# Kernel optimization log

Measured on AMD Instinct MI355X. Metric: run time of the kernel, lower is better.

Reference implementation:

```python
import jax, jax.numpy as jnp
import numpy as np

SEQDIM = 512      # hidden-state dim of h
EMBED_DIM = 512   # attention embedding dim
VFEAT_DIM = 384   # visual feature channels (must equal VFEAT_LEN for the broadcast in the original code)
VFEAT_LEN = 384   # number of visual regions


def setup_inputs() -> dict:
    key = jax.random.key(0)
    k_h, k_v, k_wh, k_wv, k_wg = jax.random.split(key, 5)
    h = jax.random.normal(k_h, (SEQDIM, 1), dtype=jnp.float32)
    v = jax.random.normal(k_v, (VFEAT_DIM, VFEAT_LEN), dtype=jnp.float32)
    wh = jax.random.normal(k_wh, (VFEAT_LEN, EMBED_DIM), dtype=jnp.float32) * 0.05
    wv = jax.random.normal(k_wv, (EMBED_DIM, VFEAT_DIM), dtype=jnp.float32) * 0.05
    wg = jax.random.normal(k_wg, (EMBED_DIM, SEQDIM), dtype=jnp.float32) * 0.05
    return {"h": h, "v": v, "wh": wh, "wv": wv, "wg": wg}


def reference(h, v, wh, wv, wg):
    # s = W_v V + (W_g h_t) 1^T  -> (embed_dim, vfeat_len)
    s = jnp.matmul(wv, v) + jnp.matmul(wg, h)  # (E, L) + (E, 1) broadcasts == outer product with ones row
    # z = w_h tanh(s)            -> (vfeat_len, vfeat_len)
    z = jnp.matmul(wh, jnp.tanh(s))
    alpha = jax.nn.softmax(z, axis=-1)
    # v (D, L) * alpha[..., None] (L, L, 1) -> broadcast to (L, D, L) with D == L
    weighted_avg = v * alpha[..., None]
    return weighted_avg
```

## Files before the change

### kernel.cpp

```cpp
#include <hip/hip_runtime.h>
#include <hip/hip_bf16.h>

#define SDIM 512
#define EDIM 512
#define LDIM 384
#define DDIM 384

typedef __attribute__((ext_vector_type(4))) float float4v;

__global__ __launch_bounds__(384) void k_tanh_s(
    const float* __restrict__ h, const float* __restrict__ v,
    const float* __restrict__ wv, const float* __restrict__ wg,
    float* __restrict__ t)
{
    const int e0  = blockIdx.x * 2;
    const int tid = threadIdx.x;
    __shared__ float wvs0[DDIM], wvs1[DDIM];
    __shared__ float red[2][6];

    float g0 = 0.f, g1 = 0.f;
    for (int k = tid; k < SDIM; k += 384) {
        const float hk = h[k];
        g0 += wg[e0 * SDIM + k] * hk;
        g1 += wg[(e0 + 1) * SDIM + k] * hk;
    }
    for (int off = 32; off > 0; off >>= 1) {
        g0 += __shfl_down(g0, off, 64);
        g1 += __shfl_down(g1, off, 64);
    }
    if ((tid & 63) == 0) { red[0][tid >> 6] = g0; red[1][tid >> 6] = g1; }

    wvs0[tid] = wv[e0 * DDIM + tid];
    wvs1[tid] = wv[(e0 + 1) * DDIM + tid];
    __syncthreads();

    const float gh0 = ((red[0][0] + red[0][1]) + (red[0][2] + red[0][3]))
                      + (red[0][4] + red[0][5]);
    const float gh1 = ((red[1][0] + red[1][1]) + (red[1][2] + red[1][3]))
                      + (red[1][4] + red[1][5]);

    const float* vp = v + tid;
    float a[4] = {0.f, 0.f, 0.f, 0.f};
    float b[4] = {0.f, 0.f, 0.f, 0.f};
    for (int kb = 0; kb < DDIM; kb += 16) {
        float vv[16];
        #pragma unroll
        for (int u = 0; u < 16; ++u)
            vv[u] = vp[(kb + u) * LDIM];
        #pragma unroll
        for (int u = 0; u < 16; ++u) {
            a[u & 3] += wvs0[kb + u] * vv[u];
            b[u & 3] += wvs1[kb + u] * vv[u];
        }
    }
    t[e0 * LDIM + tid]       = tanhf((a[0] + a[1]) + (a[2] + a[3]) + gh0);
    t[(e0 + 1) * LDIM + tid] = tanhf((b[0] + b[1]) + (b[2] + b[3]) + gh1);
}

__global__ __launch_bounds__(384) void k_softmax(
    const float* __restrict__ wh, const float* __restrict__ t,
    float* __restrict__ alpha)
{
    const int r0  = blockIdx.x * 2;
    const int tid = threadIdx.x;
    __shared__ float whs0[EDIM], whs1[EDIM];
    __shared__ float redm[2][6], reds[2][6];

    for (int e = tid; e < EDIM; e += 384) {
        whs0[e] = wh[r0 * EDIM + e];
        whs1[e] = wh[(r0 + 1) * EDIM + e];
    }
    __syncthreads();

    const float* tp = t + tid;
    float a[4] = {0.f, 0.f, 0.f, 0.f};
    float b[4] = {0.f, 0.f, 0.f, 0.f};
    for (int eb = 0; eb < EDIM; eb += 16) {
        float tv[16];
        #pragma unroll
        for (int u = 0; u < 16; ++u)
            tv[u] = tp[(eb + u) * LDIM];
        #pragma unroll
        for (int u = 0; u < 16; ++u) {
            a[u & 3] += whs0[eb + u] * tv[u];
            b[u & 3] += whs1[eb + u] * tv[u];
        }
    }
    const float z0 = (a[0] + a[1]) + (a[2] + a[3]);
    const float z1 = (b[0] + b[1]) + (b[2] + b[3]);

    float m0 = z0, m1 = z1;
    for (int off = 32; off > 0; off >>= 1) {
        m0 = fmaxf(m0, __shfl_down(m0, off, 64));
        m1 = fmaxf(m1, __shfl_down(m1, off, 64));
    }
    if ((tid & 63) == 0) { redm[0][tid >> 6] = m0; redm[1][tid >> 6] = m1; }
    __syncthreads();
    m0 = fmaxf(fmaxf(fmaxf(redm[0][0], redm[0][1]), fmaxf(redm[0][2], redm[0][3])),
               fmaxf(redm[0][4], redm[0][5]));
    m1 = fmaxf(fmaxf(fmaxf(redm[1][0], redm[1][1]), fmaxf(redm[1][2], redm[1][3])),
               fmaxf(redm[1][4], redm[1][5]));

    const float e0 = expf(z0 - m0);
    const float e1 = expf(z1 - m1);

    float s0 = e0, s1 = e1;
    for (int off = 32; off > 0; off >>= 1) {
        s0 += __shfl_down(s0, off, 64);
        s1 += __shfl_down(s1, off, 64);
    }
    if ((tid & 63) == 0) { reds[0][tid >> 6] = s0; reds[1][tid >> 6] = s1; }
    __syncthreads();
    const float rs0 = 1.f / (((reds[0][0] + reds[0][1]) + (reds[0][2] + reds[0][3]))
                             + (reds[0][4] + reds[0][5]));
    const float rs1 = 1.f / (((reds[1][0] + reds[1][1]) + (reds[1][2] + reds[1][3]))
                             + (reds[1][4] + reds[1][5]));

    alpha[r0 * LDIM + tid]       = e0 * rs0;
    alpha[(r0 + 1) * LDIM + tid] = e1 * rs1;
}

__global__ __launch_bounds__(256) void k_out(
    const float* __restrict__ v, const float* __restrict__ alpha,
    float* __restrict__ out)
{
    constexpr int VPS = (LDIM * DDIM) / 4;
    const int jt = blockIdx.x & 15;
    const int it = blockIdx.x >> 4;
    const int j0 = jt * 24;
    const int i0 = it * 16;
    const int tid = (int)threadIdx.x;

    __shared__ float al[16][24];
    for (int x = tid; x < 16 * 24; x += 256) {
        const int ii = x / 24;
        const int jj = x - ii * 24;
        al[ii][jj] = alpha[(i0 + ii) * LDIM + j0 + jj];
    }

    const float4v* v4 = (const float4v*)v;
    float4v vr[9];
    int jj[9];
    #pragma unroll
    for (int k = 0; k < 9; ++k) {
        const int x = k * 256 + tid;
        vr[k] = v4[j0 * 96 + x];
        jj[k] = x / 96;
    }
    __syncthreads();

    float4v* o4 = (float4v*)out;
    size_t base = (size_t)i0 * VPS + j0 * 96;
    for (int ii = 0; ii < 16; ++ii) {
        #pragma unroll
        for (int k = 0; k < 9; ++k)
            o4[base + k * 256 + tid] = vr[k] * al[ii][jj[k]];
        base += VPS;
    }
}

extern "C" void kernel_launch(void* const* d_in, const int* in_sizes, int n_in,
                              void* d_out, int out_size, void* d_ws, size_t ws_size,
                              hipStream_t stream)
{
    const float* h  = (const float*)d_in[0];
    const float* v  = (const float*)d_in[1];
    const float* wh = (const float*)d_in[2];
    const float* wv = (const float*)d_in[3];
    const float* wg = (const float*)d_in[4];
    float* out = (float*)d_out;

    float* t     = (float*)d_ws;
    float* alpha = t + EDIM * LDIM;

    k_tanh_s <<<EDIM / 2, 384, 0, stream>>>(h, v, wv, wg, t);
    k_softmax<<<LDIM / 2, 384, 0, stream>>>(wh, t, alpha);
    k_out    <<<16 * 24, 256, 0, stream>>>(v, alpha, out);
}
```

Before: 262.0 us.

## Fuse softmax row computation into output broadcast kernel

Merges the softmax kernel and the output kernel. Each block now recomputes one alpha row in shared memory and writes half of that row's output slab. This removes one launch and the round trip of alpha through global memory. In exchange, each row's z and softmax are computed twice, once per half, and v is re-read from global memory or cache for every output element instead of being held in registers across 16 rows.

```diff
diff --git a/kernel.cpp b/kernel.cpp
--- a/kernel.cpp
+++ b/kernel.cpp
@@ -57,105 +57,67 @@
     t[(e0 + 1) * LDIM + tid] = tanhf((b[0] + b[1]) + (b[2] + b[3]) + gh1);
 }
 
-__global__ __launch_bounds__(384) void k_softmax(
+__global__ __launch_bounds__(384) void k_fused_out(
     const float* __restrict__ wh, const float* __restrict__ t,
-    float* __restrict__ alpha)
+    const float* __restrict__ v, float* __restrict__ out)
 {
-    const int r0  = blockIdx.x * 2;
-    const int tid = threadIdx.x;
-    __shared__ float whs0[EDIM], whs1[EDIM];
-    __shared__ float redm[2][6], reds[2][6];
+    constexpr int VPS = (LDIM * DDIM) / 4;
+    const int i   = blockIdx.x >> 1;
+    const int hlf = blockIdx.x & 1;
+    const int tid = (int)threadIdx.x;
 
-    for (int e = tid; e < EDIM; e += 384) {
-        whs0[e] = wh[r0 * EDIM + e];
-        whs1[e] = wh[(r0 + 1) * EDIM + e];
-    }
+    __shared__ float whs[EDIM];
+    __shared__ float al[LDIM];
+    __shared__ float redm[6], reds[6];
+
+    for (int e = tid; e < EDIM; e += 384)
+        whs[e] = wh[i * EDIM + e];
     __syncthreads();
 
     const float* tp = t + tid;
     float a[4] = {0.f, 0.f, 0.f, 0.f};
-    float b[4] = {0.f, 0.f, 0.f, 0.f};
     for (int eb = 0; eb < EDIM; eb += 16) {
         float tv[16];
         #pragma unroll
         for (int u = 0; u < 16; ++u)
             tv[u] = tp[(eb + u) * LDIM];
         #pragma unroll
-        for (int u = 0; u < 16; ++u) {
-            a[u & 3] += whs0[eb + u] * tv[u];
-            b[u & 3] += whs1[eb + u] * tv[u];
-        }
+        for (int u = 0; u < 16; ++u)
+            a[u & 3] += whs[eb + u] * tv[u];
     }
-    const float z0 = (a[0] + a[1]) + (a[2] + a[3]);
-    const float z1 = (b[0] + b[1]) + (b[2] + b[3]);
+    const float z = (a[0] + a[1]) + (a[2] + a[3]);
 
-    float m0 = z0, m1 = z1;
-    for (int off = 32; off > 0; off >>= 1) {
-        m0 = fmaxf(m0, __shfl_down(m0, off, 64));
-        m1 = fmaxf(m1, __shfl_down(m1, off, 64));
-    }
-    if ((tid & 63) == 0) { redm[0][tid >> 6] = m0; redm[1][tid >> 6] = m1; }
+    float m = z;
+    for (int off = 32; off > 0; off >>= 1)
+        m = fmaxf(m, __shfl_down(m, off, 64));
+    if ((tid & 63) == 0) redm[tid >> 6] = m;
     __syncthreads();
-    m0 = fmaxf(fmaxf(fmaxf(redm[0][0], redm[0][1]), fmaxf(redm[0][2], redm[0][3])),
-               fmaxf(redm[0][4], redm[0][5]));
-    m1 = fmaxf(fmaxf(fmaxf(redm[1][0], redm[1][1]), fmaxf(redm[1][2], redm[1][3])),
-               fmaxf(redm[1][4], redm[1][5]));
+    m = fmaxf(fmaxf(fmaxf(redm[0], redm[1]), fmaxf(redm[2], redm[3])),
+              fmaxf(redm[4], redm[5]));
 
-    const float e0 = expf(z0 - m0);
-    const float e1 = expf(z1 - m1);
+    const float ez = expf(z - m);
+    float s = ez;
+    for (int off = 32; off > 0; off >>= 1)
+        s += __shfl_down(s, off, 64);
+    if ((tid & 63) == 0) reds[tid >> 6] = s;
+    __syncthreads();
+    const float rs = 1.f / (((reds[0] + reds[1]) + (reds[2] + reds[3]))
+                            + (reds[4] + reds[5]));
+    al[tid] = ez * rs;
+    __syncthreads();
 
-    float s0 = e0, s1 = e1;
-    for (int off = 32; off > 0; off >>= 1) {
-        s0 += __shfl_down(s0, off, 64);
-        s1 += __shfl_down(s1, off, 64);
-    }
-    if ((tid & 63) == 0) { reds[0][tid >> 6] = s0; reds[1][tid >> 6] = s1; }
-    __syncthreads();
-    const float rs0 = 1.f / (((reds[0][0] + reds[0][1]) + (reds[0][2] + reds[0][3]))
-                             + (reds[0][4] + reds[0][5]));
-    const float rs1 = 1.f / (((reds[1][0] + reds[1][1]) + (reds[1][2] + reds[1][3]))
-                             + (reds[1][4] + reds[1][5]));
-
-    alpha[r0 * LDIM + tid]       = e0 * rs0;
-    alpha[(r0 + 1) * LDIM + tid] = e1 * rs1;
-}
-
-__global__ __launch_bounds__(256) void k_out(
-    const float* __restrict__ v, const float* __restrict__ alpha,
-    float* __restrict__ out)
-{
-    constexpr int VPS = (LDIM * DDIM) / 4;
-    const int jt = blockIdx.x & 15;
-    const int it = blockIdx.x >> 4;
-    const int j0 = jt * 24;
-    const int i0 = it * 16;
-    const int tid = (int)threadIdx.x;
-
-    __shared__ float al[16][24];
-    for (int x = tid; x < 16 * 24; x += 256) {
-        const int ii = x / 24;
-        const int jj = x - ii * 24;
-        al[ii][jj] = alpha[(i0 + ii) * LDIM + j0 + jj];
-    }
+    const int jb  = tid / 96;
+    const int col = tid - jb * 96;
+    const int j0  = hlf * (LDIM / 2);
 
     const float4v* v4 = (const float4v*)v;
-    float4v vr[9];
-    int jj[9];
-    #pragma unroll
-    for (int k = 0; k < 9; ++k) {
-        const int x = k * 256 + tid;
-        vr[k] = v4[j0 * 96 + x];
-        jj[k] = x / 96;
-    }
-    __syncthreads();
+    float4v* o4 = (float4v*)out + (size_t)i * VPS;
 
-    float4v* o4 = (float4v*)out;
-    size_t base = (size_t)i0 * VPS + j0 * 96;
-    for (int ii = 0; ii < 16; ++ii) {
-        #pragma unroll
-        for (int k = 0; k < 9; ++k)
-            o4[base + k * 256 + tid] = vr[k] * al[ii][jj[k]];
-        base += VPS;
+    #pragma unroll 8
+    for (int it = 0; it < 48; ++it) {
+        const int j   = j0 + it * 4 + jb;
+        const int idx = j * 96 + col;
+        o4[idx] = v4[idx] * al[j];
     }
 }
 
@@ -170,10 +132,8 @@
     const float* wg = (const float*)d_in[4];
     float* out = (float*)d_out;
 
-    float* t     = (float*)d_ws;
-    float* alpha = t + EDIM * LDIM;
+    float* t = (float*)d_ws;
 
-    k_tanh_s <<<EDIM / 2, 384, 0, stream>>>(h, v, wv, wg, t);
-    k_softmax<<<LDIM / 2, 384, 0, stream>>>(wh, t, alpha);
-    k_out    <<<16 * 24, 256, 0, stream>>>(v, alpha, out);
+    k_tanh_s   <<<EDIM / 2, 384, 0, stream>>>(h, v, wv, wg, t);
+    k_fused_out<<<2 * LDIM, 384, 0, stream>>>(wh, t, v, out);
 }
```

Measured after the change: 263.5 us. No clear change (+0.6%).
